# Performance work log

Measured on AMD Instinct MI355X. Metric: run time of the kernel, lower is better.

Reference implementation:

```python
import jax, jax.numpy as jnp
import numpy as np

BSZ, NLVL, E, H, FFN = 8, 4, 512, 8, 2048
D = E // H
NNZ = 131072
LMAX = NNZ // BSZ  # equal per-batch counts -> static padded length
THETA = 10.0


def _layernorm(x, g, b):
    mu = x.mean(-1, keepdims=True)
    var = ((x - mu) ** 2).mean(-1, keepdims=True)
    return (x - mu) / jnp.sqrt(var + 1e-5) * g + b


def _rope(x, pos, freqs):
    # x: [N, E], pos: [N] float, freqs: [H, D/2] -> rotate interleaved pairs per head
    N = x.shape[0]
    nh, half = freqs.shape
    xr = x.reshape(N, nh, half, 2)
    ang = pos[:, None, None] * freqs[None]            # [N, H, D/2]
    c, s = jnp.cos(ang), jnp.sin(ang)
    x1, x2 = xr[..., 0], xr[..., 1]
    out = jnp.stack([x1 * c - x2 * s, x1 * s + x2 * c], axis=-1)
    return out.reshape(N, -1)


def setup_inputs() -> dict:
    key = jax.random.key(0)
    ks = jax.random.split(key, 8)
    bg = jax.random.normal(ks[0], (BSZ, NLVL, E), jnp.float32)
    feature_values = jax.random.normal(ks[1], (NNZ, E), jnp.float32)
    # coalesced sparse COO -> batch indices sorted; equal counts per batch for static shapes
    feature_batch_idx = (jnp.arange(NNZ, dtype=jnp.int32) // LMAX)
    feature_level_idx = jax.random.randint(ks[2], (NNZ,), 0, NLVL, dtype=jnp.int32)
    s = 1.0 / np.sqrt(E)
    Wq = jax.random.normal(ks[3], (E, E), jnp.float32) * s
    Wkv = jax.random.normal(ks[4], (E, 2 * E), jnp.float32) * s
    Wo = jax.random.normal(ks[5], (E, E), jnp.float32) * s
    freqs = THETA ** (-jnp.arange(D // 2, dtype=jnp.float32) * 2.0 / D)
    rope_freqs = jnp.tile(freqs[None, :], (H, 1))  # share_heads=False: per-head table
    ln_attn_g, ln_attn_b = jnp.ones(E, jnp.float32), jnp.zeros(E, jnp.float32)
    ln_ffn_g, ln_ffn_b = jnp.ones(E, jnp.float32), jnp.zeros(E, jnp.float32)
    W1 = jax.random.normal(ks[6], (E, FFN), jnp.float32) * s
    b1 = jnp.zeros(FFN, jnp.float32)
    W2 = jax.random.normal(ks[7], (FFN, E), jnp.float32) * (1.0 / np.sqrt(FFN))
    b2 = jnp.zeros(E, jnp.float32)
    return {
        'bg': bg, 'feature_values': feature_values,
        'feature_batch_idx': feature_batch_idx, 'feature_level_idx': feature_level_idx,
        'Wq': Wq, 'Wkv': Wkv, 'Wo': Wo, 'rope_freqs': rope_freqs,
        'ln_attn_g': ln_attn_g, 'ln_attn_b': ln_attn_b,
        'ln_ffn_g': ln_ffn_g, 'ln_ffn_b': ln_ffn_b,
        'W1': W1, 'b1': b1, 'W2': W2, 'b2': b2,
        'max_len': LMAX,
    }


def reference(bg, feature_values, feature_batch_idx, feature_level_idx,
              Wq, Wkv, Wo, rope_freqs, ln_attn_g, ln_attn_b,
              ln_ffn_g, ln_ffn_b, W1, b1, W2, b2, max_len):
    bsz, nlvl, e = bg.shape
    nh = rope_freqs.shape[0]
    d = e // nh
    nnz = feature_values.shape[0]

    # --- attention block (pre-norm) ---
    residual = bg
    x = _layernorm(bg, ln_attn_g, ln_attn_b)
    q = (x @ Wq).reshape(bsz * nlvl, e)
    kv = feature_values @ Wkv
    k, v = kv[:, :e], kv[:, e:]

    # RoPE on level indices (replicates original's repeat_interleave ordering: level = i // bsz)
    q_lvl = (jnp.arange(bsz * nlvl) // bsz).astype(jnp.float32)
    q = _rope(q, q_lvl, rope_freqs)
    k = _rope(k, feature_level_idx.astype(jnp.float32), rope_freqs)

    # concatenated (ragged) -> padded per batch
    counts = jax.ops.segment_sum(jnp.ones(nnz, jnp.int32), feature_batch_idx, num_segments=bsz)
    offsets = jnp.concatenate([jnp.zeros(1, jnp.int32), jnp.cumsum(counts)[:-1].astype(jnp.int32)])
    pos = jnp.arange(nnz, dtype=jnp.int32) - offsets[feature_batch_idx]
    k_pad = jnp.zeros((bsz, max_len, e), k.dtype).at[feature_batch_idx, pos].set(k)
    v_pad = jnp.zeros((bsz, max_len, e), v.dtype).at[feature_batch_idx, pos].set(v)
    pad_mask = jnp.arange(max_len)[None, :] >= counts[:, None]  # True at padding

    # SDPA
    qh = q.reshape(bsz, nlvl, nh, d).transpose(0, 2, 1, 3)
    kh = k_pad.reshape(bsz, max_len, nh, d).transpose(0, 2, 1, 3)
    vh = v_pad.reshape(bsz, max_len, nh, d).transpose(0, 2, 1, 3)
    scores = jnp.einsum('bhqd,bhkd->bhqk', qh, kh) / jnp.sqrt(jnp.asarray(d, qh.dtype))
    scores = jnp.where(pad_mask[:, None, None, :], -jnp.inf, scores)
    attn = jax.nn.softmax(scores, axis=-1)
    o = jnp.einsum('bhqk,bhkd->bhqd', attn, vh).transpose(0, 2, 1, 3).reshape(bsz, nlvl, e)
    o = o @ Wo + residual

    # --- FFN block (pre-norm) ---
    y = _layernorm(o, ln_ffn_g, ln_ffn_b)
    y = jax.nn.relu(y @ W1 + b1) @ W2 + b2
    return o + y
```

## Files before the change

kernel.cpp:

```cpp
#include <hip/hip_runtime.h>
#include <hip/hip_bf16.h>
#include <math.h>

#define BSZ 8
#define NLVL 4
#define E 512
#define H 8
#define D 64
#define FFN 2048
#define NNZ 131072
#define NQ 32
#define P32 32
#define NEGF -3.0e38f

typedef __attribute__((ext_vector_type(8))) short bf16x8;
typedef __attribute__((ext_vector_type(4))) float f32x4;

#define WS_QROT   16
#define WS_WSUM   (WS_QROT + NQ*E)
#define WS_OATT   (WS_WSUM + BSZ*P32*E)
#define WS_O2     (WS_OATT + NQ*E)
#define WS_Y      (WS_O2 + NQ*E)
#define WS_HID    (WS_Y + NQ*E)
#define WS_PART   (WS_HID + NQ*FFN)
#define WS_ML     (WS_PART + 512*P32*E)
#define WS_WALL   (WS_ML + 512*P32*2)

__device__ inline short f2bf(float x) {
    __hip_bfloat16 h = __float2bfloat16(x);
    union { __hip_bfloat16 v; short s; } u; u.v = h; return u.s;
}

__global__ void k_zero(int* wsi) {
    if (blockIdx.x == 0 && threadIdx.x < 8) wsi[threadIdx.x] = 0;
}

__global__ void k_hist(const int* __restrict__ fb, int* wsi) {
    __shared__ int h[8];
    int t = threadIdx.x;
    if (t < 8) h[t] = 0;
    __syncthreads();
    for (int j = blockIdx.x * 256 + t; j < NNZ; j += gridDim.x * 256)
        atomicAdd(&h[fb[j]], 1);
    __syncthreads();
    if (t < 8) atomicAdd(&wsi[t], h[t]);
}

__global__ void k_off(int* wsi) {
    if (threadIdx.x == 0) {
        int run = 0;
        for (int b = 0; b < 8; b++) { wsi[8 + b] = run; run += wsi[b]; }
    }
}

__global__ void k_qrot(const float* __restrict__ bg, const float* __restrict__ Wq,
                       const float* __restrict__ rf, const float* __restrict__ g,
                       const float* __restrict__ bb, float* __restrict__ ws) {
    __shared__ float xr[E];
    __shared__ float qrow[E];
    __shared__ float red[8];
    int r = blockIdx.x, t = threadIdx.x;
    float v0 = bg[r * E + t], v1 = bg[r * E + t + 256];
    float s = v0 + v1;
    for (int o = 32; o > 0; o >>= 1) s += __shfl_down(s, o, 64);
    if ((t & 63) == 0) red[t >> 6] = s;
    __syncthreads();
    if (t == 0) red[0] = (red[0] + red[1] + red[2] + red[3]) * (1.0f / E);
    __syncthreads();
    float mu = red[0];
    __syncthreads();
    float d0 = v0 - mu, d1 = v1 - mu;
    s = d0 * d0 + d1 * d1;
    for (int o = 32; o > 0; o >>= 1) s += __shfl_down(s, o, 64);
    if ((t & 63) == 0) red[t >> 6] = s;
    __syncthreads();
    if (t == 0) red[0] = rsqrtf((red[0] + red[1] + red[2] + red[3]) * (1.0f / E) + 1e-5f);
    __syncthreads();
    float rstd = red[0];
    xr[t] = d0 * rstd * g[t] + bb[t];
    xr[t + 256] = d1 * rstd * g[t + 256] + bb[t + 256];
    __syncthreads();
    for (int half = 0; half < 2; half++) {
        int c = t + half * 256;
        float acc = 0.f;
        for (int e = 0; e < E; e++) acc += xr[e] * Wq[e * E + c];
        qrow[c] = acc;
    }
    __syncthreads();
    int c0 = 2 * t, c1 = c0 + 1;
    int h = c0 >> 6, ii = (c0 & 63) >> 1;
    float freq = rf[h * 32 + ii];
    float pos = (float)(r >> 3);
    float a = pos * freq, ca = cosf(a), sa = sinf(a);
    float x1 = qrow[c0], x2 = qrow[c1];
    float* qr = ws + WS_QROT + r * E;
    qr[c0] = x1 * ca - x2 * sa;
    qr[c1] = x1 * sa + x2 * ca;
}

__global__ void k_wtil(const float* __restrict__ Wkv, const float* __restrict__ rf,
                       const float* __restrict__ ws, short* __restrict__ wall) {
    __shared__ float u[D];
    int blk = blockIdx.x;
    int h = blk & 7, lvl = (blk >> 3) & 3, r = blk >> 5;
    int b = r >> 2, l = r & 3;
    int t = threadIdx.x;
    const float* qr = ws + WS_QROT + r * E + h * D;
    if (t < 32) {
        float freq = rf[h * 32 + t];
        float a = (float)lvl * freq;
        float ca = cosf(a), sa = sinf(a);
        float x1 = qr[2 * t], x2 = qr[2 * t + 1];
        u[2 * t] = x1 * ca + x2 * sa;
        u[2 * t + 1] = -x1 * sa + x2 * ca;
    }
    __syncthreads();
    int n = lvl * 32 + l * 8 + h;
    short* wrow_out = wall + ((size_t)(b * 128 + n)) * E;
    for (int rep = 0; rep < 8; rep++) {
        int e = t + rep * 64;
        const float* wrow = Wkv + (size_t)e * (2 * E) + h * D;
        float acc = 0.f;
#pragma unroll
        for (int c = 0; c < D; c++) acc += wrow[c] * u[c];
        wrow_out[e] = f2bf(acc * 0.125f);
    }
}

#define KSTR 520
#define TSTR 40
__global__ __launch_bounds__(256, 2) void k_flash(
    const float* __restrict__ fv, const int* __restrict__ fl,
    const short* __restrict__ wall, const int* __restrict__ wsi,
    const int* __restrict__ maxlen, float* __restrict__ part, float* __restrict__ ml) {
    __shared__ short kbuf[32 * KSTR];
    __shared__ short fvT[512 * TSTR];
    __shared__ short pbuf[32 * TSTR];
    __shared__ float mbuf[4 * 32];
    __shared__ float lpart[4 * 32];
    __shared__ float alph[32];
    __shared__ float mrun[32];
    __shared__ float lrun[32];

    int t = threadIdx.x;
    int w = t >> 6, lane = t & 63, col = lane & 15, quad = lane >> 4;
    int b = blockIdx.x, kc = blockIdx.y;
    int cnt = wsi[b], mlen = maxlen[0];
    int lim = cnt < mlen ? cnt : mlen;
    int off = wsi[8 + b];
    int kbase = kc * 256;
    int nv = lim - kbase; if (nv > 256) nv = 256; if (nv < 0) nv = 0;

    if (t < 32) { mrun[t] = NEGF; lrun[t] = 0.f; }

    f32x4 acc_o[2][8];
#pragma unroll
    for (int mt = 0; mt < 2; mt++)
#pragma unroll
        for (int nt = 0; nt < 8; nt++) acc_o[mt][nt] = f32x4{0.f, 0.f, 0.f, 0.f};

    const short* wallb = wall + (size_t)b * 128 * E;
    int sj = (t & 15) * 2;
    int se = (t >> 4) * 32;

    for (int s = 0; s < 8; s++) {
        int vs = nv - s * 32;
        if (vs <= 0) break;
        __syncthreads();
        {
            int g0 = off + kbase + s * 32 + sj;
            int g1 = g0 + 1;
            if (g0 > NNZ - 1) g0 = NNZ - 1;
            if (g1 > NNZ - 1) g1 = NNZ - 1;
            const float* r0 = fv + (size_t)g0 * E + se;
            const float* r1 = fv + (size_t)g1 * E + se;
#pragma unroll
            for (int i = 0; i < 8; i++) {
                float4 x0 = *(const float4*)(r0 + i * 4);
                float4 x1 = *(const float4*)(r1 + i * 4);
                int e = se + i * 4;
                *(__hip_bfloat162*)&kbuf[sj * KSTR + e]       = __float22bfloat162_rn(float2{x0.x, x0.y});
                *(__hip_bfloat162*)&kbuf[sj * KSTR + e + 2]   = __float22bfloat162_rn(float2{x0.z, x0.w});
                *(__hip_bfloat162*)&kbuf[(sj+1) * KSTR + e]   = __float22bfloat162_rn(float2{x1.x, x1.y});
                *(__hip_bfloat162*)&kbuf[(sj+1) * KSTR + e+2] = __float22bfloat162_rn(float2{x1.z, x1.w});
                *(__hip_bfloat162*)&fvT[(e + 0) * TSTR + sj] = __float22bfloat162_rn(float2{x0.x, x1.x});
                *(__hip_bfloat162*)&fvT[(e + 1) * TSTR + sj] = __float22bfloat162_rn(float2{x0.y, x1.y});
                *(__hip_bfloat162*)&fvT[(e + 2) * TSTR + sj] = __float22bfloat162_rn(float2{x0.z, x1.z});
                *(__hip_bfloat162*)&fvT[(e + 3) * TSTR + sj] = __float22bfloat162_rn(float2{x0.w, x1.w});
            }
        }
        __syncthreads();
        f32x4 acc_s[2][2];
#pragma unroll
        for (int mt = 0; mt < 2; mt++)
#pragma unroll
            for (int kt = 0; kt < 2; kt++) acc_s[mt][kt] = f32x4{0.f, 0.f, 0.f, 0.f};
        {
            const short* wr0 = wallb + (size_t)(w * 32 + col) * E + quad * 8;
            const short* wr1 = wr0 + (size_t)16 * E;
            const short* kb0 = &kbuf[col * KSTR + quad * 8];
            const short* kb1 = &kbuf[(16 + col) * KSTR + quad * 8];
#pragma unroll
            for (int ks = 0; ks < 16; ks++) {
                int e0 = ks * 32;
                bf16x8 A0 = *(const bf16x8*)(wr0 + e0);
                bf16x8 A1 = *(const bf16x8*)(wr1 + e0);
                bf16x8 B0 = *(const bf16x8*)(kb0 + e0);
                bf16x8 B1 = *(const bf16x8*)(kb1 + e0);
                acc_s[0][0] = __builtin_amdgcn_mfma_f32_16x16x32_bf16(A0, B0, acc_s[0][0], 0, 0, 0);
                acc_s[0][1] = __builtin_amdgcn_mfma_f32_16x16x32_bf16(A0, B1, acc_s[0][1], 0, 0, 0);
                acc_s[1][0] = __builtin_amdgcn_mfma_f32_16x16x32_bf16(A1, B0, acc_s[1][0], 0, 0, 0);
                acc_s[1][1] = __builtin_amdgcn_mfma_f32_16x16x32_bf16(A1, B1, acc_s[1][1], 0, 0, 0);
            }
        }
        int kg0 = off + kbase + s * 32 + col;
        int kg1 = kg0 + 16;
        if (kg0 > NNZ - 1) kg0 = NNZ - 1;
        if (kg1 > NNZ - 1) kg1 = NNZ - 1;
        int lv0 = fl[kg0], lv1 = fl[kg1];
        bool valid0 = (s * 32 + col) < nv;
        bool valid1 = (s * 32 + 16 + col) < nv;
        bool sel0 = valid0 && (lv0 == w);
        bool sel1 = valid1 && (lv1 == w);
#pragma unroll
        for (int mt = 0; mt < 2; mt++) {
#pragma unroll
            for (int r = 0; r < 4; r++) {
                float v0 = sel0 ? acc_s[mt][0][r] : NEGF;
                float v1 = sel1 ? acc_s[mt][1][r] : NEGF;
                float v = fmaxf(v0, v1);
#pragma unroll
                for (int msk = 1; msk < 16; msk <<= 1) v = fmaxf(v, __shfl_xor(v, msk, 16));
                if (col == 0) mbuf[w * 32 + mt * 16 + quad * 4 + r] = v;
            }
        }
        __syncthreads();
        if (t < 32) {
            int p = t;
            float mo = mrun[p];
            float mn = mo;
            mn = fmaxf(mn, mbuf[p]);
            mn = fmaxf(mn, mbuf[32 + p]);
            mn = fmaxf(mn, mbuf[64 + p]);
            mn = fmaxf(mn, mbuf[96 + p]);
            alph[p] = expf(mo - mn);
            mrun[p] = mn;
        }
        __syncthreads();
        float mr[2][4], ar[2][4];
#pragma unroll
        for (int mt = 0; mt < 2; mt++)
#pragma unroll
            for (int r = 0; r < 4; r++) {
                int p = mt * 16 + quad * 4 + r;
                mr[mt][r] = mrun[p];
                ar[mt][r] = alph[p];
            }
#pragma unroll
        for (int mt = 0; mt < 2; mt++) {
#pragma unroll
            for (int r = 0; r < 4; r++) {
                int p = mt * 16 + quad * 4 + r;
                float ls = 0.f;
                {
                    if (sel0) {
                        float pv = expf(acc_s[mt][0][r] - mr[mt][r]);
                        pbuf[p * TSTR + col] = f2bf(pv);
                        ls += pv;
                    } else if (w == 0 && !valid0) {
                        pbuf[p * TSTR + col] = 0;
                    }
                    if (sel1) {
                        float pv = expf(acc_s[mt][1][r] - mr[mt][r]);
                        pbuf[p * TSTR + 16 + col] = f2bf(pv);
                        ls += pv;
                    } else if (w == 0 && !valid1) {
                        pbuf[p * TSTR + 16 + col] = 0;
                    }
                }
#pragma unroll
                for (int msk = 1; msk < 16; msk <<= 1) ls += __shfl_xor(ls, msk, 16);
                if (col == 0) lpart[w * 32 + p] = ls;
            }
        }
#pragma unroll
        for (int mt = 0; mt < 2; mt++)
#pragma unroll
            for (int nt = 0; nt < 8; nt++)
#pragma unroll
                for (int r = 0; r < 4; r++) acc_o[mt][nt][r] *= ar[mt][r];
        __syncthreads();
        {
            bf16x8 Ap0 = *(const bf16x8*)&pbuf[col * TSTR + quad * 8];
            bf16x8 Ap1 = *(const bf16x8*)&pbuf[(16 + col) * TSTR + quad * 8];
            const short* bt = &fvT[(size_t)(w * 128 + col) * TSTR + quad * 8];
#pragma unroll
            for (int nt = 0; nt < 8; nt++) {
                bf16x8 Bf = *(const bf16x8*)(bt + (size_t)nt * 16 * TSTR);
                acc_o[0][nt] = __builtin_amdgcn_mfma_f32_16x16x32_bf16(Ap0, Bf, acc_o[0][nt], 0, 0, 0);
                acc_o[1][nt] = __builtin_amdgcn_mfma_f32_16x16x32_bf16(Ap1, Bf, acc_o[1][nt], 0, 0, 0);
            }
        }
        if (t < 32) {
            int p = t;
            lrun[p] = lrun[p] * alph[p] + (lpart[p] + lpart[32 + p] + lpart[64 + p] + lpart[96 + p]);
        }
    }
    size_t pbase = ((size_t)(b * 64 + kc) * P32) * E;
#pragma unroll
    for (int mt = 0; mt < 2; mt++)
#pragma unroll
        for (int r = 0; r < 4; r++) {
            int p = mt * 16 + quad * 4 + r;
#pragma unroll
            for (int nt = 0; nt < 8; nt++) {
                int e = w * 128 + nt * 16 + col;
                part[pbase + (size_t)p * E + e] = acc_o[mt][nt][r];
            }
        }
    if (t < 32) {
        size_t idx = (size_t)(b * 64 + kc) * P32 + t;
        ml[idx * 2] = mrun[t];
        ml[idx * 2 + 1] = lrun[t];
    }
}

__global__ void k_merge(const float* __restrict__ part, const float* __restrict__ ml,
                        float* __restrict__ wsum) {
    __shared__ float wexp[64];
    int b = blockIdx.x >> 5, p = blockIdx.x & 31;
    int t = threadIdx.x;
    float M = NEGF;
    for (int kc = 0; kc < 64; kc++)
        M = fmaxf(M, ml[((size_t)(b * 64 + kc) * P32 + p) * 2]);
    float denom = 0.f;
    for (int kc = 0; kc < 64; kc++) {
        size_t idx = ((size_t)(b * 64 + kc) * P32 + p) * 2;
        denom += ml[idx + 1] * expf(ml[idx] - M);
    }
    if (t < 64)
        wexp[t] = expf(ml[((size_t)(b * 64 + t) * P32 + p) * 2] - M);
    __syncthreads();
    float inv = 1.0f / denom;
    for (int half = 0; half < 2; half++) {
        int e = t + half * 256;
        float acc = 0.f;
        for (int kc = 0; kc < 64; kc++)
            acc += part[((size_t)(b * 64 + kc) * P32 + p) * E + e] * wexp[kc];
        wsum[((size_t)(b * P32 + p)) * E + e] = acc * inv;
    }
}

__global__ void k_oproj(const float* __restrict__ wsum, const float* __restrict__ Wkv,
                        float* __restrict__ oatt) {
    __shared__ float Aw[NQ][E];
    int h = blockIdx.x >> 2, ct = blockIdx.x & 3;
    int t = threadIdx.x;
    {
        int rr = t >> 3, x = (t & 7) * 64;
        int row = (rr >> 2) * P32 + (rr & 3) * 8 + h;
#pragma unroll
        for (int q4 = 0; q4 < 16; q4++)
            *(float4*)&Aw[rr][x + q4 * 4] = *(const float4*)&wsum[(size_t)row * E + x + q4 * 4];
    }
    __syncthreads();
#pragma unroll
    for (int rep = 0; rep < 2; rep++) {
        int idx = rep * 256 + t;
        int rr = idx >> 4, cl = idx & 15;
        int c = h * D + ct * 16 + cl;
        float acc = 0.f;
        for (int e = 0; e < E; e++) acc += Aw[rr][e] * Wkv[(size_t)e * (2 * E) + E + c];
        oatt[rr * E + c] = acc;
    }
}

__global__ void k_wo(const float* __restrict__ oatt, const float* __restrict__ Wo,
                     const float* __restrict__ bg, float* __restrict__ o2) {
    __shared__ float Aw[NQ * E];
    int t = threadIdx.x;
#pragma unroll
    for (int q = 0; q < 16; q++) {
        int i = (q * 256 + t) * 4;
        *(float4*)&Aw[i] = *(const float4*)&oatt[i];
    }
    __syncthreads();
    int ct = blockIdx.x;
#pragma unroll
    for (int rep = 0; rep < 4; rep++) {
        int idx = rep * 256 + t;
        int rr = idx >> 5, cl = idx & 31;
        int c = ct * 32 + cl;
        float acc = bg[rr * E + c];
        for (int e = 0; e < E; e++) acc += Aw[rr * E + e] * Wo[(size_t)e * E + c];
        o2[rr * E + c] = acc;
    }
}

__global__ void k_ln2(const float* __restrict__ o2, const float* __restrict__ g,
                      const float* __restrict__ bb, float* __restrict__ y) {
    __shared__ float red[8];
    int r = blockIdx.x, t = threadIdx.x;
    float v0 = o2[r * E + t], v1 = o2[r * E + t + 256];
    float s = v0 + v1;
    for (int o = 32; o > 0; o >>= 1) s += __shfl_down(s, o, 64);
    if ((t & 63) == 0) red[t >> 6] = s;
    __syncthreads();
    if (t == 0) red[0] = (red[0] + red[1] + red[2] + red[3]) * (1.0f / E);
    __syncthreads();
    float mu = red[0];
    __syncthreads();
    float d0 = v0 - mu, d1 = v1 - mu;
    s = d0 * d0 + d1 * d1;
    for (int o = 32; o > 0; o >>= 1) s += __shfl_down(s, o, 64);
    if ((t & 63) == 0) red[t >> 6] = s;
    __syncthreads();
    if (t == 0) red[0] = rsqrtf((red[0] + red[1] + red[2] + red[3]) * (1.0f / E) + 1e-5f);
    __syncthreads();
    float rstd = red[0];
    y[r * E + t] = d0 * rstd * g[t] + bb[t];
    y[r * E + t + 256] = d1 * rstd * g[t + 256] + bb[t + 256];
}

__global__ void k_ffn1(const float* __restrict__ y, const float* __restrict__ W1,
                       const float* __restrict__ b1, float* __restrict__ hid) {
    __shared__ float Aw[NQ * E];
    int t = threadIdx.x;
#pragma unroll
    for (int q = 0; q < 16; q++) {
        int i = (q * 256 + t) * 4;
        *(float4*)&Aw[i] = *(const float4*)&y[i];
    }
    __syncthreads();
    int ft = blockIdx.x;
#pragma unroll
    for (int rep = 0; rep < 4; rep++) {
        int idx = rep * 256 + t;
        int rr = idx >> 5, fl = idx & 31;
        int f = ft * 32 + fl;
        float acc = b1[f];
        for (int e = 0; e < E; e++) acc += Aw[rr * E + e] * W1[(size_t)e * FFN + f];
        hid[rr * FFN + f] = fmaxf(acc, 0.f);
    }
}

__global__ void k_ffn2(const float* __restrict__ hid, const float* __restrict__ W2,
                       const float* __restrict__ b2, const float* __restrict__ o2,
                       float* __restrict__ out) {
    int ct = blockIdx.x;
    int t = threadIdx.x;
#pragma unroll
    for (int rep = 0; rep < 2; rep++) {
        int idx = rep * 256 + t;
        int rr = idx >> 4, cl = idx & 15;
        int c = ct * 16 + cl;
        float acc = b2[c] + o2[rr * E + c];
        for (int f = 0; f < FFN; f++) acc += hid[rr * FFN + f] * W2[(size_t)f * E + c];
        out[rr * E + c] = acc;
    }
}

extern "C" void kernel_launch(void* const* d_in, const int* in_sizes, int n_in,
                              void* d_out, int out_size, void* d_ws, size_t ws_size,
                              hipStream_t stream) {
    const float* bg  = (const float*)d_in[0];
    const float* fv  = (const float*)d_in[1];
    const int*   fb  = (const int*)d_in[2];
    const int*   fl  = (const int*)d_in[3];
    const float* Wq  = (const float*)d_in[4];
    const float* Wkv = (const float*)d_in[5];
    const float* Wo  = (const float*)d_in[6];
    const float* rf  = (const float*)d_in[7];
    const float* lag = (const float*)d_in[8];
    const float* lab = (const float*)d_in[9];
    const float* lfg = (const float*)d_in[10];
    const float* lfb = (const float*)d_in[11];
    const float* W1  = (const float*)d_in[12];
    const float* b1  = (const float*)d_in[13];
    const float* W2  = (const float*)d_in[14];
    const float* b2  = (const float*)d_in[15];
    const int* maxlen = (const int*)d_in[16];
    float* ws = (float*)d_ws;
    int* wsi = (int*)d_ws;
    short* wall = (short*)(ws + WS_WALL);
    float* out = (float*)d_out;

    hipLaunchKernelGGL(k_zero, dim3(1), dim3(64), 0, stream, wsi);
    hipLaunchKernelGGL(k_hist, dim3(128), dim3(256), 0, stream, fb, wsi);
    hipLaunchKernelGGL(k_off, dim3(1), dim3(64), 0, stream, wsi);
    hipLaunchKernelGGL(k_qrot, dim3(NQ), dim3(256), 0, stream, bg, Wq, rf, lag, lab, ws);
    hipLaunchKernelGGL(k_wtil, dim3(NQ * NLVL * H), dim3(64), 0, stream, Wkv, rf, ws, wall);
    hipLaunchKernelGGL(k_flash, dim3(BSZ, 64), dim3(256), 0, stream,
                       fv, fl, wall, wsi, maxlen, ws + WS_PART, ws + WS_ML);
    hipLaunchKernelGGL(k_merge, dim3(BSZ * P32), dim3(256), 0, stream,
                       ws + WS_PART, ws + WS_ML, ws + WS_WSUM);
    hipLaunchKernelGGL(k_oproj, dim3(H * 4), dim3(256), 0, stream,
                       ws + WS_WSUM, Wkv, ws + WS_OATT);
    hipLaunchKernelGGL(k_wo, dim3(16), dim3(256), 0, stream,
                       ws + WS_OATT, Wo, bg, ws + WS_O2);
    hipLaunchKernelGGL(k_ln2, dim3(NQ), dim3(256), 0, stream,
                       ws + WS_O2, lfg, lfb, ws + WS_Y);
    hipLaunchKernelGGL(k_ffn1, dim3(FFN / 32), dim3(256), 0, stream,
                       ws + WS_Y, W1, b1, ws + WS_HID);
    hipLaunchKernelGGL(k_ffn2, dim3(E / 16), dim3(256), 0, stream,
                       ws + WS_HID, W2, b2, ws + WS_O2, out);
}
```

Before: 864.8 us.

## Prefetch next feature tile in registers, keep softmax stats in registers, transpose Wkv

The flash-attention kernel now loads the next 32-row chunk of feature values into registers while the current chunk is converted and used, so global load latency overlaps compute. Running max and sum stay in per-lane registers instead of shared memory, which removes one barrier per step and switches expf to the faster __expf. MFMA sections get raised wave priority. A new transpose kernel writes Wkv into the partial-result workspace so k_wtil reads it with coalesced loads. The cost is higher register pressure from the prefetch buffers, plus reliance on the workspace region being free before k_flash overwrites it.

Measured after the change: 861.7 us. About the same (-0.4%).

```diff
diff --git a/kernel.cpp b/kernel.cpp
--- a/kernel.cpp
+++ b/kernel.cpp
@@ -50,6 +50,24 @@
     if (threadIdx.x == 0) {
         int run = 0;
         for (int b = 0; b < 8; b++) { wsi[8 + b] = run; run += wsi[b]; }
+    }
+}
+
+__global__ void k_tr(const float* __restrict__ Wkv, float* __restrict__ wkt) {
+    __shared__ float tile[64][65];
+    int ct = blockIdx.x & 7, et = blockIdx.x >> 3;
+    int t = threadIdx.x;
+    int tc = t & 63, tr = t >> 6;
+#pragma unroll
+    for (int i = 0; i < 16; i++) {
+        int e = et * 64 + tr + i * 4;
+        tile[tr + i * 4][tc] = Wkv[(size_t)e * (2 * E) + ct * 64 + tc];
+    }
+    __syncthreads();
+#pragma unroll
+    for (int i = 0; i < 16; i++) {
+        int c = tr + i * 4;
+        wkt[(size_t)(ct * 64 + c) * E + et * 64 + tc] = tile[tc][c];
     }
 }
 
@@ -98,7 +116,7 @@
     qr[c1] = x1 * sa + x2 * ca;
 }
 
-__global__ void k_wtil(const float* __restrict__ Wkv, const float* __restrict__ rf,
+__global__ void k_wtil(const float* __restrict__ wkt, const float* __restrict__ rf,
                        const float* __restrict__ ws, short* __restrict__ wall) {
     __shared__ float u[D];
     int blk = blockIdx.x;
@@ -115,16 +133,19 @@
         u[2 * t + 1] = -x1 * sa + x2 * ca;
     }
     __syncthreads();
+    float acc[8];
+#pragma unroll
+    for (int i = 0; i < 8; i++) acc[i] = 0.f;
+    for (int c = 0; c < D; c++) {
+        float uc = u[c];
+        const float* wt = wkt + (size_t)(h * D + c) * E + t;
+#pragma unroll
+        for (int i = 0; i < 8; i++) acc[i] += wt[i * 64] * uc;
+    }
     int n = lvl * 32 + l * 8 + h;
     short* wrow_out = wall + ((size_t)(b * 128 + n)) * E;
-    for (int rep = 0; rep < 8; rep++) {
-        int e = t + rep * 64;
-        const float* wrow = Wkv + (size_t)e * (2 * E) + h * D;
-        float acc = 0.f;
-#pragma unroll
-        for (int c = 0; c < D; c++) acc += wrow[c] * u[c];
-        wrow_out[e] = f2bf(acc * 0.125f);
-    }
+#pragma unroll
+    for (int i = 0; i < 8; i++) wrow_out[t + i * 64] = f2bf(acc[i] * 0.125f);
 }
 
 #define KSTR 520
@@ -138,9 +159,6 @@
     __shared__ short pbuf[32 * TSTR];
     __shared__ float mbuf[4 * 32];
     __shared__ float lpart[4 * 32];
-    __shared__ float alph[32];
-    __shared__ float mrun[32];
-    __shared__ float lrun[32];
 
     int t = threadIdx.x;
     int w = t >> 6, lane = t & 63, col = lane & 15, quad = lane >> 4;
@@ -151,7 +169,11 @@
     int kbase = kc * 256;
     int nv = lim - kbase; if (nv > 256) nv = 256; if (nv < 0) nv = 0;
 
-    if (t < 32) { mrun[t] = NEGF; lrun[t] = 0.f; }
+    float m_reg[2][4], l_reg[2][4], a_reg[2][4];
+#pragma unroll
+    for (int mt = 0; mt < 2; mt++)
+#pragma unroll
+        for (int r = 0; r < 4; r++) { m_reg[mt][r] = NEGF; l_reg[mt][r] = 0.f; }
 
     f32x4 acc_o[2][8];
 #pragma unroll
@@ -162,33 +184,59 @@
     const short* wallb = wall + (size_t)b * 128 * E;
     int sj = (t & 15) * 2;
     int se = (t >> 4) * 32;
+
+    float4 pf0[8], pf1[8];
+    if (nv > 0) {
+        int g0 = off + kbase + sj, g1 = g0 + 1;
+        if (g0 > NNZ - 1) g0 = NNZ - 1;
+        if (g1 > NNZ - 1) g1 = NNZ - 1;
+        const float* r0 = fv + (size_t)g0 * E + se;
+        const float* r1 = fv + (size_t)g1 * E + se;
+#pragma unroll
+        for (int i = 0; i < 8; i++) {
+            pf0[i] = *(const float4*)(r0 + i * 4);
+            pf1[i] = *(const float4*)(r1 + i * 4);
+        }
+    }
 
     for (int s = 0; s < 8; s++) {
         int vs = nv - s * 32;
         if (vs <= 0) break;
         __syncthreads();
-        {
-            int g0 = off + kbase + s * 32 + sj;
-            int g1 = g0 + 1;
+#pragma unroll
+        for (int i = 0; i < 8; i++) {
+            float4 x0 = pf0[i], x1 = pf1[i];
+            int e = se + i * 4;
+            *(__hip_bfloat162*)&kbuf[sj * KSTR + e]           = __float22bfloat162_rn(float2{x0.x, x0.y});
+            *(__hip_bfloat162*)&kbuf[sj * KSTR + e + 2]       = __float22bfloat162_rn(float2{x0.z, x0.w});
+            *(__hip_bfloat162*)&kbuf[(sj + 1) * KSTR + e]     = __float22bfloat162_rn(float2{x1.x, x1.y});
+            *(__hip_bfloat162*)&kbuf[(sj + 1) * KSTR + e + 2] = __float22bfloat162_rn(float2{x1.z, x1.w});
+            *(__hip_bfloat162*)&fvT[(e + 0) * TSTR + sj] = __float22bfloat162_rn(float2{x0.x, x1.x});
+            *(__hip_bfloat162*)&fvT[(e + 1) * TSTR + sj] = __float22bfloat162_rn(float2{x0.y, x1.y});
+            *(__hip_bfloat162*)&fvT[(e + 2) * TSTR + sj] = __float22bfloat162_rn(float2{x0.z, x1.z});
+            *(__hip_bfloat162*)&fvT[(e + 3) * TSTR + sj] = __float22bfloat162_rn(float2{x0.w, x1.w});
+        }
+        if (nv - (s + 1) * 32 > 0) {
+            int g0 = off + kbase + (s + 1) * 32 + sj, g1 = g0 + 1;
             if (g0 > NNZ - 1) g0 = NNZ - 1;
             if (g1 > NNZ - 1) g1 = NNZ - 1;
             const float* r0 = fv + (size_t)g0 * E + se;
             const float* r1 = fv + (size_t)g1 * E + se;
 #pragma unroll
             for (int i = 0; i < 8; i++) {
-                float4 x0 = *(const float4*)(r0 + i * 4);
-                float4 x1 = *(const float4*)(r1 + i * 4);
-                int e = se + i * 4;
-                *(__hip_bfloat162*)&kbuf[sj * KSTR + e]       = __float22bfloat162_rn(float2{x0.x, x0.y});
-                *(__hip_bfloat162*)&kbuf[sj * KSTR + e + 2]   = __float22bfloat162_rn(float2{x0.z, x0.w});
-                *(__hip_bfloat162*)&kbuf[(sj+1) * KSTR + e]   = __float22bfloat162_rn(float2{x1.x, x1.y});
-                *(__hip_bfloat162*)&kbuf[(sj+1) * KSTR + e+2] = __float22bfloat162_rn(float2{x1.z, x1.w});
-                *(__hip_bfloat162*)&fvT[(e + 0) * TSTR + sj] = __float22bfloat162_rn(float2{x0.x, x1.x});
-                *(__hip_bfloat162*)&fvT[(e + 1) * TSTR + sj] = __float22bfloat162_rn(float2{x0.y, x1.y});
-                *(__hip_bfloat162*)&fvT[(e + 2) * TSTR + sj] = __float22bfloat162_rn(float2{x0.z, x1.z});
-                *(__hip_bfloat162*)&fvT[(e + 3) * TSTR + sj] = __float22bfloat162_rn(float2{x0.w, x1.w});
-            }
-        }
+                pf0[i] = *(const float4*)(r0 + i * 4);
+                pf1[i] = *(const float4*)(r1 + i * 4);
+            }
+        }
+        int kg0 = off + kbase + s * 32 + col;
+        int kg1 = kg0 + 16;
+        if (kg0 > NNZ - 1) kg0 = NNZ - 1;
+        if (kg1 > NNZ - 1) kg1 = NNZ - 1;
+        int lv0 = fl[kg0], lv1 = fl[kg1];
+        bool valid0 = (s * 32 + col) < nv;
+        bool valid1 = (s * 32 + 16 + col) < nv;
+        bool sel0 = valid0 && (lv0 == w);
+        bool sel1 = valid1 && (lv1 == w);
         __syncthreads();
         f32x4 acc_s[2][2];
 #pragma unroll
@@ -200,6 +248,7 @@
             const short* wr1 = wr0 + (size_t)16 * E;
             const short* kb0 = &kbuf[col * KSTR + quad * 8];
             const short* kb1 = &kbuf[(16 + col) * KSTR + quad * 8];
+            __builtin_amdgcn_s_setprio(1);
 #pragma unroll
             for (int ks = 0; ks < 16; ks++) {
                 int e0 = ks * 32;
@@ -212,16 +261,8 @@
                 acc_s[1][0] = __builtin_amdgcn_mfma_f32_16x16x32_bf16(A1, B0, acc_s[1][0], 0, 0, 0);
                 acc_s[1][1] = __builtin_amdgcn_mfma_f32_16x16x32_bf16(A1, B1, acc_s[1][1], 0, 0, 0);
             }
-        }
-        int kg0 = off + kbase + s * 32 + col;
-        int kg1 = kg0 + 16;
-        if (kg0 > NNZ - 1) kg0 = NNZ - 1;
-        if (kg1 > NNZ - 1) kg1 = NNZ - 1;
-        int lv0 = fl[kg0], lv1 = fl[kg1];
-        bool valid0 = (s * 32 + col) < nv;
-        bool valid1 = (s * 32 + 16 + col) < nv;
-        bool sel0 = valid0 && (lv0 == w);
-        bool sel1 = valid1 && (lv1 == w);
+            __builtin_amdgcn_s_setprio(0);
+        }
 #pragma unroll
         for (int mt = 0; mt < 2; mt++) {
 #pragma unroll
@@ -235,26 +276,16 @@
             }
         }
         __syncthreads();
-        if (t < 32) {
-            int p = t;
-            float mo = mrun[p];
-            float mn = mo;
-            mn = fmaxf(mn, mbuf[p]);
-            mn = fmaxf(mn, mbuf[32 + p]);
-            mn = fmaxf(mn, mbuf[64 + p]);
-            mn = fmaxf(mn, mbuf[96 + p]);
-            alph[p] = expf(mo - mn);
-            mrun[p] = mn;
-        }
-        __syncthreads();
-        float mr[2][4], ar[2][4];
 #pragma unroll
         for (int mt = 0; mt < 2; mt++)
 #pragma unroll
             for (int r = 0; r < 4; r++) {
                 int p = mt * 16 + quad * 4 + r;
-                mr[mt][r] = mrun[p];
-                ar[mt][r] = alph[p];
+                float mo = m_reg[mt][r];
+                float mn = fmaxf(mo, fmaxf(fmaxf(mbuf[p], mbuf[32 + p]),
+                                           fmaxf(mbuf[64 + p], mbuf[96 + p])));
+                a_reg[mt][r] = __expf(mo - mn);
+                m_reg[mt][r] = mn;
             }
 #pragma unroll
         for (int mt = 0; mt < 2; mt++) {
@@ -262,21 +293,19 @@
             for (int r = 0; r < 4; r++) {
                 int p = mt * 16 + quad * 4 + r;
                 float ls = 0.f;
-                {
-                    if (sel0) {
-                        float pv = expf(acc_s[mt][0][r] - mr[mt][r]);
-                        pbuf[p * TSTR + col] = f2bf(pv);
-                        ls += pv;
-                    } else if (w == 0 && !valid0) {
-                        pbuf[p * TSTR + col] = 0;
-                    }
-                    if (sel1) {
-                        float pv = expf(acc_s[mt][1][r] - mr[mt][r]);
-                        pbuf[p * TSTR + 16 + col] = f2bf(pv);
-                        ls += pv;
-                    } else if (w == 0 && !valid1) {
-                        pbuf[p * TSTR + 16 + col] = 0;
-                    }
+                if (sel0) {
+                    float pv = __expf(acc_s[mt][0][r] - m_reg[mt][r]);
+                    pbuf[p * TSTR + col] = f2bf(pv);
+                    ls += pv;
+                } else if (w == 0 && !valid0) {
+                    pbuf[p * TSTR + col] = 0;
+                }
+                if (sel1) {
+                    float pv = __expf(acc_s[mt][1][r] - m_reg[mt][r]);
+                    pbuf[p * TSTR + 16 + col] = f2bf(pv);
+                    ls += pv;
+                } else if (w == 0 && !valid1) {
+                    pbuf[p * TSTR + 16 + col] = 0;
                 }
 #pragma unroll
                 for (int msk = 1; msk < 16; msk <<= 1) ls += __shfl_xor(ls, msk, 16);
@@ -288,23 +317,29 @@
 #pragma unroll
             for (int nt = 0; nt < 8; nt++)
 #pragma unroll
-                for (int r = 0; r < 4; r++) acc_o[mt][nt][r] *= ar[mt][r];
+                for (int r = 0; r < 4; r++) acc_o[mt][nt][r] *= a_reg[mt][r];
         __syncthreads();
         {
             bf16x8 Ap0 = *(const bf16x8*)&pbuf[col * TSTR + quad * 8];
             bf16x8 Ap1 = *(const bf16x8*)&pbuf[(16 + col) * TSTR + quad * 8];
             const short* bt = &fvT[(size_t)(w * 128 + col) * TSTR + quad * 8];
+            __builtin_amdgcn_s_setprio(1);
 #pragma unroll
             for (int nt = 0; nt < 8; nt++) {
                 bf16x8 Bf = *(const bf16x8*)(bt + (size_t)nt * 16 * TSTR);
                 acc_o[0][nt] = __builtin_amdgcn_mfma_f32_16x16x32_bf16(Ap0, Bf, acc_o[0][nt], 0, 0, 0);
                 acc_o[1][nt] = __builtin_amdgcn_mfma_f32_16x16x32_bf16(Ap1, Bf, acc_o[1][nt], 0, 0, 0);
             }
-        }
-        if (t < 32) {
-            int p = t;
-            lrun[p] = lrun[p] * alph[p] + (lpart[p] + lpart[32 + p] + lpart[64 + p] + lpart[96 + p]);
-        }
+            __builtin_amdgcn_s_setprio(0);
+        }
+#pragma unroll
+        for (int mt = 0; mt < 2; mt++)
+#pragma unroll
+            for (int r = 0; r < 4; r++) {
+                int p = mt * 16 + quad * 4 + r;
+                l_reg[mt][r] = l_reg[mt][r] * a_reg[mt][r] +
+                               (lpart[p] + lpart[32 + p] + lpart[64 + p] + lpart[96 + p]);
+            }
     }
     size_t pbase = ((size_t)(b * 64 + kc) * P32) * E;
 #pragma unroll
@@ -318,10 +353,16 @@
                 part[pbase + (size_t)p * E + e] = acc_o[mt][nt][r];
             }
         }
-    if (t < 32) {
-        size_t idx = (size_t)(b * 64 + kc) * P32 + t;
-        ml[idx * 2] = mrun[t];
-        ml[idx * 2 + 1] = lrun[t];
+    if (w == 0 && col == 0) {
+#pragma unroll
+        for (int mt = 0; mt < 2; mt++)
+#pragma unroll
+            for (int r = 0; r < 4; r++) {
+                int p = mt * 16 + quad * 4 + r;
+                size_t idx = (size_t)(b * 64 + kc) * P32 + p;
+                ml[idx * 2] = m_reg[mt][r];
+                ml[idx * 2 + 1] = l_reg[mt][r];
+            }
     }
 }
 
@@ -483,13 +524,15 @@
     float* ws = (float*)d_ws;
     int* wsi = (int*)d_ws;
     short* wall = (short*)(ws + WS_WALL);
+    float* wkt = ws + WS_PART;
     float* out = (float*)d_out;
 
     hipLaunchKernelGGL(k_zero, dim3(1), dim3(64), 0, stream, wsi);
     hipLaunchKernelGGL(k_hist, dim3(128), dim3(256), 0, stream, fb, wsi);
     hipLaunchKernelGGL(k_off, dim3(1), dim3(64), 0, stream, wsi);
+    hipLaunchKernelGGL(k_tr, dim3(64), dim3(256), 0, stream, Wkv, wkt);
     hipLaunchKernelGGL(k_qrot, dim3(NQ), dim3(256), 0, stream, bg, Wq, rf, lag, lab, ws);
-    hipLaunchKernelGGL(k_wtil, dim3(NQ * NLVL * H), dim3(64), 0, stream, Wkv, rf, ws, wall);
+    hipLaunchKernelGGL(k_wtil, dim3(NQ * NLVL * H), dim3(64), 0, stream, wkt, rf, ws, wall);
     hipLaunchKernelGGL(k_flash, dim3(BSZ, 64), dim3(256), 0, stream,
                        fv, fl, wall, wsi, maxlen, ws + WS_PART, ws + WS_ML);
     hipLaunchKernelGGL(k_merge, dim3(BSZ * P32), dim3(256), 0, stream,
```
